# Optimization experiments

Hardware: AMD Instinct MI355X
Metric: run time of the kernel (lower is better)

Reference implementation:

```python
import jax, jax.numpy as jnp
import numpy as np

B, T, E, H, NT, NC = 256, 512, 200, 100, 100000, 5


def setup_inputs() -> dict:
    key = jax.random.key(0)
    ks = jax.random.split(key, 16)
    w = lambda i, shape: jax.random.normal(ks[i], shape, dtype=jnp.float32) * 0.05
    return {
        "txt": jax.random.randint(ks[0], (B, T), 0, NT),
        "lens": jax.random.randint(ks[1], (B,), 1, T + 1),
        "emb": w(2, (NT, E)),
        "W_ih": w(3, (3 * H, E)), "W_hh": w(4, (3 * H, H)),
        "b_ih": w(5, (3 * H,)), "b_hh": w(6, (3 * H,)),
        "W_lgr": w(7, (1, 2 * H)), "b_lgr": w(8, (1,)),
        "W_ts": w(9, (H, H)), "b_ts": w(10, (H,)),
        "W_ti": w(11, (H, H)), "b_ti": w(12, (H,)),
        "W_out": w(13, (NC, H)), "b_out": w(14, (NC,)),
    }


def reference(txt, lens, emb, W_ih, W_hh, b_ih, b_hh, W_lgr, b_lgr,
              W_ts, b_ts, W_ti, b_ti, W_out, b_out):
    bsz = txt.shape[0]
    # Embedding lookup with max_norm=1 renorm (torch nn.Embedding max_norm semantics)
    rows = emb[txt]  # (B,T,E)
    n = jnp.linalg.norm(rows, axis=-1, keepdims=True)
    emb_w = rows * jnp.where(n > 1.0, 1.0 / (n + 1e-7), 1.0)
    # eval mode: dropout is identity

    # ---- single-layer GRU (batch_first), gates in torch order r,z,n ----
    xp = emb_w @ W_ih.T + b_ih  # (B,T,3H), input projections precomputed

    def gru_step(h, x):
        hp = h @ W_hh.T + b_hh
        xr, xz, xn = jnp.split(x, 3, axis=-1)
        hr, hz, hn = jnp.split(hp, 3, axis=-1)
        r = jax.nn.sigmoid(xr + hr)
        z = jax.nn.sigmoid(xz + hz)
        ng = jnp.tanh(xn + r * hn)
        h = (1.0 - z) * ng + z * h
        return h, h

    h0 = jnp.zeros((bsz, H), jnp.float32)
    _, hs = jax.lax.scan(gru_step, h0, jnp.swapaxes(xp, 0, 1))
    rnn_out = jnp.swapaxes(hs, 0, 1)  # (B,T,H)

    # ---- cosine attention against an all-ones query ----
    inn = rnn_out / jnp.maximum(jnp.linalg.norm(rnn_out, axis=-1, keepdims=True), 1e-12)
    q = jnp.ones((bsz, H), jnp.float32)
    qn = q / jnp.maximum(jnp.linalg.norm(q, axis=-1, keepdims=True), 1e-12)
    att = jnp.einsum('bth,bh->bt', inn, qn) / H
    mask = (jnp.arange(T)[None, :] < lens[:, None]).astype(att.dtype)
    a_w = att * mask  # (B,T)

    # ---- gated-state recurrence ----
    z_all = jax.nn.relu(a_w)[..., None]          # (B,T,1)
    ti = rnn_out @ W_ti.T + b_ti                  # (B,T,H) trans_inp precomputed
    lgr_in = rnn_out @ W_lgr[:, :H].T             # (B,T,1) input half of lgr
    Wls = W_lgr[:, H:]                            # state half of lgr

    def rec_step(state, xs):
        ti_t, li_t, z_t = xs
        gate = jax.nn.sigmoid(li_t + state @ Wls.T + b_lgr)
        ns = jnp.tanh(ti_t + (gate * state) @ W_ts.T + b_ts)
        state = (1.0 - z_t) * state + z_t * ns
        return state, None

    xs = (jnp.swapaxes(ti, 0, 1), jnp.swapaxes(lgr_in, 0, 1), jnp.swapaxes(z_all, 0, 1))
    state, _ = jax.lax.scan(rec_step, jnp.zeros((bsz, H), jnp.float32), xs)
    return state @ W_out.T + b_out  # (B,NC)
```

## Files before the change

### kernel.cpp

```cpp
#include <hip/hip_runtime.h>

#define B_   256
#define T_   512
#define E_   200
#define H_   100
#define H3_  300
#define NC_  5

#define WSTRIDE 304

__device__ __forceinline__ void fma4(float4& acc, float a, const float4& w) {
    acc.x = fmaf(a, w.x, acc.x);
    acc.y = fmaf(a, w.y, acc.y);
    acc.z = fmaf(a, w.z, acc.z);
    acc.w = fmaf(a, w.w, acc.w);
}

#define KEEP4(v) asm volatile("" : "+v"((v).x), "+v"((v).y), "+v"((v).z), "+v"((v).w))

__device__ __forceinline__ void ldsbar() {
    asm volatile("s_waitcnt lgkmcnt(0)" ::: "memory");
    __builtin_amdgcn_s_barrier();
    __builtin_amdgcn_sched_barrier(0);
}

__global__ void k_pack(const float* __restrict__ W_ih, const float* __restrict__ W_ti,
                       const float* __restrict__ W_lgr,
                       float* __restrict__ wT, float* __restrict__ wcat) {
    int idx = blockIdx.x * 256 + threadIdx.x;
    if (idx < E_ * H3_) {
        int k = idx / H3_, j = idx - k * H3_;
        wT[idx] = W_ih[j * E_ + k];
    }
    int i2 = idx - E_ * H3_;
    if (i2 >= 0 && i2 < H_ * 104) {
        int k = i2 / 104, j = i2 - k * 104;
        float v = 0.0f;
        if (j < H_) v = W_ti[j * H_ + k];
        else if (j == H_) v = W_lgr[k];
        wcat[i2] = v;
    }
}

__global__ __launch_bounds__(320) void k_embgemm(
        const int* __restrict__ txt, const float* __restrict__ emb,
        const float* __restrict__ wT, const float* __restrict__ b_ih,
        float* __restrict__ xp) {
    __shared__ __align__(16) float A_lds[E_ * 36];
    __shared__ __align__(16) float W_lds[2][16 * WSTRIDE];
    __shared__ float pp_lds[10][32];
    __shared__ float scale_lds[32];

    int tid = threadIdx.x;
    int base = blockIdx.x * 32;

#pragma unroll
    for (int L = 0; L < 5; ++L) {
        int q = tid + 320 * L;
        int r = q / 50, k4 = q % 50;
        int row = txt[base + r];
        float4 v = ((const float4*)(emb + (size_t)row * E_))[k4];
        int k = k4 * 4;
        A_lds[(k + 0) * 36 + r] = v.x;
        A_lds[(k + 1) * 36 + r] = v.y;
        A_lds[(k + 2) * 36 + r] = v.z;
        A_lds[(k + 3) * 36 + r] = v.w;
    }
#pragma unroll
    for (int L = 0; L < 4; ++L) {
        int f = tid + 320 * L;
        if (f < 16 * 75) {
            int kl = f / 75, j4 = f % 75;
            float4 v = ((const float4*)wT)[kl * 75 + j4];
            *(float4*)&W_lds[0][kl * WSTRIDE + j4 * 4] = v;
        }
    }
    __syncthreads();

    {
        int r = tid % 32, s = tid / 32;
        float ss = 0.f;
        for (int k = s * 20; k < s * 20 + 20; ++k) {
            float v = A_lds[k * 36 + r];
            ss = fmaf(v, v, ss);
        }
        pp_lds[s][r] = ss;
    }
    __syncthreads();
    if (tid < 32) {
        float ss = 0.f;
#pragma unroll
        for (int s = 0; s < 10; ++s) ss += pp_lds[s][tid];
        float n = sqrtf(ss);
        scale_lds[tid] = (n > 1.0f) ? (1.0f / (n + 1e-7f)) : 1.0f;
    }

    int c = tid % 80, g = tid / 80;
    float4 acc[8];
#pragma unroll
    for (int i = 0; i < 8; ++i) acc[i] = make_float4(0.f, 0.f, 0.f, 0.f);

    const int NT = 13;
    for (int ic = 0; ic < NT; ++ic) {
        int KC = (ic == 12) ? 8 : 16;
        int cur = ic & 1;

        float4 pf0, pf1, pf2, pf3;
        int nKC = 0;
        if (ic + 1 < NT) {
            nKC = (ic + 1 == 12) ? 8 : 16;
            const float4* src = ((const float4*)wT) + (ic + 1) * 16 * 75;
            int f0 = tid;
            if (f0 < nKC * 75) pf0 = src[f0];
            int f1 = tid + 320;
            if (f1 < nKC * 75) pf1 = src[f1];
            int f2 = tid + 640;
            if (f2 < nKC * 75) pf2 = src[f2];
            int f3 = tid + 960;
            if (f3 < nKC * 75) pf3 = src[f3];
        }

        if (c < 75) {
            for (int kk = 0; kk < KC; ++kk) {
                int k = ic * 16 + kk;
                float4 wv = *(const float4*)&W_lds[cur][kk * WSTRIDE + c * 4];
                float4 a0 = *(const float4*)&A_lds[k * 36 + g * 8];
                float4 a1 = *(const float4*)&A_lds[k * 36 + g * 8 + 4];
                fma4(acc[0], a0.x, wv); fma4(acc[1], a0.y, wv);
                fma4(acc[2], a0.z, wv); fma4(acc[3], a0.w, wv);
                fma4(acc[4], a1.x, wv); fma4(acc[5], a1.y, wv);
                fma4(acc[6], a1.z, wv); fma4(acc[7], a1.w, wv);
            }
        }

        if (ic + 1 < NT) {
            int f0 = tid;
            if (f0 < nKC * 75) *(float4*)&W_lds[cur ^ 1][(f0 / 75) * WSTRIDE + (f0 % 75) * 4] = pf0;
            int f1 = tid + 320;
            if (f1 < nKC * 75) *(float4*)&W_lds[cur ^ 1][(f1 / 75) * WSTRIDE + (f1 % 75) * 4] = pf1;
            int f2 = tid + 640;
            if (f2 < nKC * 75) *(float4*)&W_lds[cur ^ 1][(f2 / 75) * WSTRIDE + (f2 % 75) * 4] = pf2;
            int f3 = tid + 960;
            if (f3 < nKC * 75) *(float4*)&W_lds[cur ^ 1][(f3 / 75) * WSTRIDE + (f3 % 75) * 4] = pf3;
        }
        ldsbar();
    }

    if (c < 75) {
        float4 bv = *(const float4*)&b_ih[c * 4];
#pragma unroll
        for (int rr = 0; rr < 8; ++rr) {
            int r = g * 8 + rr;
            float s = scale_lds[r];
            float4 res;
            res.x = fmaf(acc[rr].x, s, bv.x);
            res.y = fmaf(acc[rr].y, s, bv.y);
            res.z = fmaf(acc[rr].z, s, bv.z);
            res.w = fmaf(acc[rr].w, s, bv.w);
            *(float4*)&xp[(size_t)(base + r) * H3_ + c * 4] = res;
        }
    }
}

__global__ __launch_bounds__(640, 3)
void k_gru(
        const float* __restrict__ xp, const float* __restrict__ W_hh,
        const float* __restrict__ b_hh, float* __restrict__ rnn) {
    __shared__ __align__(16) float h_lds[104];
    __shared__ float p_lds[640];

    int tid = threadIdx.x;
    int half = (tid >= 320) ? 1 : 0;
    int j = tid - half * 320;
    int kb = half ? 48 : 0;
    int b = blockIdx.x;

    float4 w[13];
    if (j < H3_) {
        const float4* wr = (const float4*)(W_hh + (size_t)j * H_ + kb);
#pragma unroll
        for (int i = 0; i < 13; ++i) w[i] = wr[i];
        if (half) w[0] = make_float4(0.f, 0.f, 0.f, 0.f);
#pragma unroll
        for (int i = 0; i < 13; ++i) KEEP4(w[i]);
    } else {
#pragma unroll
        for (int i = 0; i < 13; ++i) w[i] = make_float4(0.f, 0.f, 0.f, 0.f);
    }

    float bhr = 0.f, bhz = 0.f, bhn = 0.f;
    if (tid < H_) { bhr = b_hh[tid]; bhz = b_hh[H_ + tid]; bhn = b_hh[2 * H_ + tid]; }

    if (tid < 104) h_lds[tid] = 0.0f;
    float hown = 0.0f;

    const float* xpb = xp + (size_t)b * T_ * H3_;
    float* rnnb = rnn + (size_t)b * T_ * H_;
    float xr = 0.f, xz = 0.f, xn = 0.f;
    if (tid < H_) { xr = xpb[tid]; xz = xpb[H_ + tid]; xn = xpb[2 * H_ + tid]; }
    __syncthreads();

    for (int t = 0; t < T_; ++t) {
        float a0 = 0.f, a1 = 0.f, a2 = 0.f, a3 = 0.f;
#pragma unroll
        for (int i = 0; i < 13; ++i) {
            float4 hv = *(const float4*)&h_lds[kb + i * 4];
            a0 = fmaf(w[i].x, hv.x, a0);
            a1 = fmaf(w[i].y, hv.y, a1);
            a2 = fmaf(w[i].z, hv.z, a2);
            a3 = fmaf(w[i].w, hv.w, a3);
        }
        float ownp = (a0 + a1) + (a2 + a3);
        if (j < H3_) p_lds[tid] = ownp;
        float nxr = 0.f, nxz = 0.f, nxn = 0.f;
        if (tid < H_ && t + 1 < T_) {
            const float* xq = xpb + (size_t)(t + 1) * H3_;
            nxr = xq[tid]; nxz = xq[H_ + tid]; nxn = xq[2 * H_ + tid];
        }
        ldsbar();
        if (tid < H_) {
            float hr = ownp             + p_lds[320 + tid] + bhr;
            float hz = p_lds[100 + tid] + p_lds[420 + tid] + bhz;
            float hn = p_lds[200 + tid] + p_lds[520 + tid] + bhn;
            float r = 1.0f / (1.0f + expf(-(xr + hr)));
            float z = 1.0f / (1.0f + expf(-(xz + hz)));
            float ng = tanhf(xn + r * hn);
            float hnew = (1.0f - z) * ng + z * hown;
            hown = hnew;
            h_lds[tid] = hnew;
            rnnb[(size_t)t * H_ + tid] = hnew;
            xr = nxr; xz = nxz; xn = nxn;
        }
        ldsbar();
    }
}

__global__ __launch_bounds__(256) void k_post(
        const float* __restrict__ rnn, const float* __restrict__ wcat,
        const float* __restrict__ b_ti, const int* __restrict__ lens,
        float* __restrict__ ti, float* __restrict__ lgr, float* __restrict__ zr) {
    __shared__ __align__(16) float A_lds[H_ * 72];
    __shared__ __align__(16) float W_lds[H_ * 112];

    int tid = threadIdx.x;
    int base = blockIdx.x * 64;

    for (int idx = tid; idx < 64 * H_; idx += 256) {
        int r = idx / H_, k = idx - r * H_;
        A_lds[k * 72 + r] = rnn[(size_t)(base + r) * H_ + k];
    }
    for (int idx = tid; idx < H_ * 104; idx += 256) {
        int k = idx / 104, jj = idx - k * 104;
        W_lds[k * 112 + jj] = wcat[idx];
    }
    __syncthreads();

    if (tid < 64) {
        float ss = 0.f, sm = 0.f;
        for (int k = 0; k < H_; ++k) {
            float v = A_lds[k * 72 + tid];
            ss = fmaf(v, v, ss); sm += v;
        }
        int row = base + tid;
        int bb = row >> 9, tt = row & 511;
        float att = sm / (fmaxf(sqrtf(ss), 1e-12f) * 1000.0f);
        zr[row] = (tt < lens[bb]) ? fmaxf(att, 0.0f) : 0.0f;
    }

    int c = tid % 32, g = tid / 32;
    float4 acc[8];
#pragma unroll
    for (int i = 0; i < 8; ++i) acc[i] = make_float4(0.f, 0.f, 0.f, 0.f);

    if (c < 26) {
        for (int k = 0; k < H_; ++k) {
            float4 wv = *(const float4*)&W_lds[k * 112 + c * 4];
            float4 a0 = *(const float4*)&A_lds[k * 72 + g * 8];
            float4 a1 = *(const float4*)&A_lds[k * 72 + g * 8 + 4];
            fma4(acc[0], a0.x, wv); fma4(acc[1], a0.y, wv);
            fma4(acc[2], a0.z, wv); fma4(acc[3], a0.w, wv);
            fma4(acc[4], a1.x, wv); fma4(acc[5], a1.y, wv);
            fma4(acc[6], a1.z, wv); fma4(acc[7], a1.w, wv);
        }
    }

    if (c < 25) {
        float4 bv = *(const float4*)&b_ti[c * 4];
#pragma unroll
        for (int rr = 0; rr < 8; ++rr) {
            int row = base + g * 8 + rr;
            float4 res;
            res.x = acc[rr].x + bv.x; res.y = acc[rr].y + bv.y;
            res.z = acc[rr].z + bv.z; res.w = acc[rr].w + bv.w;
            *(float4*)&ti[(size_t)row * H_ + c * 4] = res;
        }
    } else if (c == 25) {
#pragma unroll
        for (int rr = 0; rr < 8; ++rr) {
            int row = base + g * 8 + rr;
            lgr[row] = acc[rr].x;
        }
    }
}

__global__ __launch_bounds__(256, 1)
void k_rec(
        const float* __restrict__ ti, const float* __restrict__ lgr,
        const float* __restrict__ zr,
        const float* __restrict__ W_ts, const float* __restrict__ b_ts,
        const float* __restrict__ W_lgr, const float* __restrict__ b_lgr,
        const float* __restrict__ W_out, const float* __restrict__ b_out,
        float* __restrict__ out) {
    __shared__ __align__(16) float sA[104];
    __shared__ __align__(16) float sB[104];
    __shared__ float p_lds[256];
    __shared__ float red[2][2];

    int tid = threadIdx.x;
    int half = (tid >= 128) ? 1 : 0;
    int j = tid - half * 128;
    int kb = half ? 48 : 0;
    int b = blockIdx.x;

    float4 w[13];
    if (j < H_) {
        const float4* wr = (const float4*)(W_ts + (size_t)j * H_ + kb);
#pragma unroll
        for (int i = 0; i < 13; ++i) w[i] = wr[i];
        if (half) w[0] = make_float4(0.f, 0.f, 0.f, 0.f);
#pragma unroll
        for (int i = 0; i < 13; ++i) KEEP4(w[i]);
    } else {
#pragma unroll
        for (int i = 0; i < 13; ++i) w[i] = make_float4(0.f, 0.f, 0.f, 0.f);
    }

    float bts = 0.f, wlj = 0.f;
    if (tid < H_) { bts = b_ts[tid]; wlj = W_lgr[H_ + tid]; }
    float blg = b_lgr[0];
    if (tid < 104) sA[tid] = 0.0f;
    if (tid < 4) ((float*)red)[tid] = 0.0f;
    float sown = 0.0f;

    size_t rb = (size_t)b * T_;
    float tiv = 0.f, zt = 0.f, lt = 0.f;
    if (tid < H_) tiv = ti[rb * H_ + tid];
    zt = zr[rb]; lt = lgr[rb];
    __syncthreads();

    float* rd = sA;
    float* wrb = sB;
    for (int t = 0; t < T_; ++t) {
        float a0 = 0.f, a1 = 0.f, a2 = 0.f, a3 = 0.f;
#pragma unroll
        for (int i = 0; i < 13; ++i) {
            float4 s4 = *(const float4*)&rd[kb + i * 4];
            a0 = fmaf(w[i].x, s4.x, a0); a1 = fmaf(w[i].y, s4.y, a1);
            a2 = fmaf(w[i].z, s4.z, a2); a3 = fmaf(w[i].w, s4.w, a3);
        }
        float ownp = (a0 + a1) + (a2 + a3);
        if (half && j < H_) p_lds[tid] = ownp;
        float ntiv = 0.f, nzt = 0.f, nlt = 0.f;
        if (t + 1 < T_) {
            if (tid < H_) ntiv = ti[(rb + t + 1) * H_ + tid];
            nzt = zr[rb + t + 1]; nlt = lgr[rb + t + 1];
        }
        ldsbar();
        float dot = red[t & 1][0] + red[t & 1][1];
        float part = 0.0f;
        if (tid < H_) {
            float sv = ownp + p_lds[128 + tid];
            float gate = 1.0f / (1.0f + expf(-(lt + dot + blg)));
            float ns = tanhf(tiv + gate * sv + bts);
            float snew = (1.0f - zt) * sown + zt * ns;
            sown = snew;
            wrb[tid] = snew;
            part = wlj * snew;
        }
        tiv = ntiv; zt = nzt; lt = nlt;
#pragma unroll
        for (int off = 1; off < 64; off <<= 1) part += __shfl_xor(part, off, 64);
        if ((tid & 63) == 0 && tid < 128) red[(t + 1) & 1][tid >> 6] = part;
        ldsbar();
        float* tmp = rd; rd = wrb; wrb = tmp;
    }

    if (tid < NC_) {
        float o = b_out[tid];
        for (int k = 0; k < H_; ++k) o = fmaf(rd[k], W_out[tid * H_ + k], o);
        out[b * NC_ + tid] = o;
    }
}

extern "C" void kernel_launch(void* const* d_in, const int* in_sizes, int n_in,
                              void* d_out, int out_size, void* d_ws, size_t ws_size,
                              hipStream_t stream) {
    const int*   txt   = (const int*)d_in[0];
    const int*   lens  = (const int*)d_in[1];
    const float* emb   = (const float*)d_in[2];
    const float* W_ih  = (const float*)d_in[3];
    const float* W_hh  = (const float*)d_in[4];
    const float* b_ih  = (const float*)d_in[5];
    const float* b_hh  = (const float*)d_in[6];
    const float* W_lgr = (const float*)d_in[7];
    const float* b_lgr = (const float*)d_in[8];
    const float* W_ts  = (const float*)d_in[9];
    const float* b_ts  = (const float*)d_in[10];
    const float* W_ti  = (const float*)d_in[11];
    const float* b_ti  = (const float*)d_in[12];
    const float* W_out = (const float*)d_in[13];
    const float* b_out = (const float*)d_in[14];

    float* ws   = (float*)d_ws;
    float* xp   = ws;
    float* rnn  = xp + 39321600;
    float* lgrv = rnn + 13107200;
    float* zrv  = lgrv + 131072;
    float* wT   = zrv + 131072;
    float* wcat = wT + 60000;
    float* ti   = xp;

    float* out = (float*)d_out;

    k_pack<<<276, 256, 0, stream>>>(W_ih, W_ti, W_lgr, wT, wcat);
    k_embgemm<<<4096, 320, 0, stream>>>(txt, emb, wT, b_ih, xp);
    k_gru<<<256, 640, 0, stream>>>(xp, W_hh, b_hh, rnn);
    k_post<<<2048, 256, 0, stream>>>(rnn, wcat, b_ti, lens, ti, lgrv, zrv);
    k_rec<<<256, 256, 0, stream>>>(ti, lgrv, zrv, W_ts, b_ts, W_lgr, b_lgr,
                                   W_out, b_out, out);
}
```

Measured before the change: 1.528 ms.

## Split GRU and recurrence dot products three ways and broadcast state via readlane

Both sequential recurrences now split the hidden-size reduction across three thread groups of 36/32/32 elements instead of two halves of roughly 52, using 960 and 384 threads per block. Each lane loads a single element of the state from LDS once per step, and the dot product pulls each operand with v_readlane as a scalar instead of doing repeated float4 LDS reads. The aim is a shorter per-step critical path in these latency-bound scans. In exchange there are more waves per barrier, a third partial sum to combine, and possible readlane hazard stalls. The k_rec state double buffer is replaced by a single LDS buffer.

```diff
diff --git a/kernel.cpp b/kernel.cpp
--- a/kernel.cpp
+++ b/kernel.cpp
@@ -22,6 +22,23 @@
     asm volatile("s_waitcnt lgkmcnt(0)" ::: "memory");
     __builtin_amdgcn_s_barrier();
     __builtin_amdgcn_sched_barrier(0);
+}
+
+__device__ __forceinline__ float rlane(float v, int l) {
+    return __uint_as_float(__builtin_amdgcn_readlane(__float_as_uint(v), (unsigned)l));
+}
+
+template<int N4>
+__device__ __forceinline__ float dotseg(const float4 (&w)[9], float hreg) {
+    float a0 = 0.f, a1 = 0.f, a2 = 0.f, a3 = 0.f;
+#pragma unroll
+    for (int q = 0; q < N4; ++q) {
+        a0 = fmaf(w[q].x, rlane(hreg, 4 * q + 0), a0);
+        a1 = fmaf(w[q].y, rlane(hreg, 4 * q + 1), a1);
+        a2 = fmaf(w[q].z, rlane(hreg, 4 * q + 2), a2);
+        a3 = fmaf(w[q].w, rlane(hreg, 4 * q + 3), a3);
+    }
+    return (a0 + a1) + (a2 + a3);
 }
 
 __global__ void k_pack(const float* __restrict__ W_ih, const float* __restrict__ W_ti,
@@ -162,56 +179,48 @@
     }
 }
 
-__global__ __launch_bounds__(640, 3)
+__global__ __launch_bounds__(960)
+__attribute__((amdgpu_waves_per_eu(1, 4)))
 void k_gru(
         const float* __restrict__ xp, const float* __restrict__ W_hh,
         const float* __restrict__ b_hh, float* __restrict__ rnn) {
-    __shared__ __align__(16) float h_lds[104];
-    __shared__ float p_lds[640];
+    __shared__ float h_lds[104];
+    __shared__ float p_lds[960];
 
     int tid = threadIdx.x;
-    int half = (tid >= 320) ? 1 : 0;
-    int j = tid - half * 320;
-    int kb = half ? 48 : 0;
+    int lane = tid & 63;
+    int third = tid / 320;
+    int j = tid - third * 320;
+    int kb = (third == 0) ? 0 : (third == 1 ? 36 : 68);
+    int seg = (third == 0) ? 36 : 32;
+    int seg4 = (third == 0) ? 9 : 8;
     int b = blockIdx.x;
 
-    float4 w[13];
+    float4 w4[9];
+#pragma unroll
+    for (int q = 0; q < 9; ++q) w4[q] = make_float4(0.f, 0.f, 0.f, 0.f);
     if (j < H3_) {
         const float4* wr = (const float4*)(W_hh + (size_t)j * H_ + kb);
 #pragma unroll
-        for (int i = 0; i < 13; ++i) w[i] = wr[i];
-        if (half) w[0] = make_float4(0.f, 0.f, 0.f, 0.f);
-#pragma unroll
-        for (int i = 0; i < 13; ++i) KEEP4(w[i]);
-    } else {
-#pragma unroll
-        for (int i = 0; i < 13; ++i) w[i] = make_float4(0.f, 0.f, 0.f, 0.f);
-    }
+        for (int q = 0; q < 9; ++q) if (q < seg4) w4[q] = wr[q];
+    }
+#pragma unroll
+    for (int q = 0; q < 9; ++q) KEEP4(w4[q]);
 
     float bhr = 0.f, bhz = 0.f, bhn = 0.f;
     if (tid < H_) { bhr = b_hh[tid]; bhz = b_hh[H_ + tid]; bhn = b_hh[2 * H_ + tid]; }
-
-    if (tid < 104) h_lds[tid] = 0.0f;
-    float hown = 0.0f;
 
     const float* xpb = xp + (size_t)b * T_ * H3_;
     float* rnnb = rnn + (size_t)b * T_ * H_;
     float xr = 0.f, xz = 0.f, xn = 0.f;
     if (tid < H_) { xr = xpb[tid]; xz = xpb[H_ + tid]; xn = xpb[2 * H_ + tid]; }
-    __syncthreads();
+
+    float hreg = 0.f;
+    float hown = 0.f;
 
     for (int t = 0; t < T_; ++t) {
-        float a0 = 0.f, a1 = 0.f, a2 = 0.f, a3 = 0.f;
-#pragma unroll
-        for (int i = 0; i < 13; ++i) {
-            float4 hv = *(const float4*)&h_lds[kb + i * 4];
-            a0 = fmaf(w[i].x, hv.x, a0);
-            a1 = fmaf(w[i].y, hv.y, a1);
-            a2 = fmaf(w[i].z, hv.z, a2);
-            a3 = fmaf(w[i].w, hv.w, a3);
-        }
-        float ownp = (a0 + a1) + (a2 + a3);
-        if (j < H3_) p_lds[tid] = ownp;
+        float p = (third == 0) ? dotseg<9>(w4, hreg) : dotseg<8>(w4, hreg);
+        if (j < H3_) p_lds[tid] = p;
         float nxr = 0.f, nxz = 0.f, nxn = 0.f;
         if (tid < H_ && t + 1 < T_) {
             const float* xq = xpb + (size_t)(t + 1) * H3_;
@@ -219,9 +228,9 @@
         }
         ldsbar();
         if (tid < H_) {
-            float hr = ownp             + p_lds[320 + tid] + bhr;
-            float hz = p_lds[100 + tid] + p_lds[420 + tid] + bhz;
-            float hn = p_lds[200 + tid] + p_lds[520 + tid] + bhn;
+            float hr = p + p_lds[320 + tid] + p_lds[640 + tid] + bhr;
+            float hz = p_lds[100 + tid] + p_lds[420 + tid] + p_lds[740 + tid] + bhz;
+            float hn = p_lds[200 + tid] + p_lds[520 + tid] + p_lds[840 + tid] + bhn;
             float r = 1.0f / (1.0f + expf(-(xr + hr)));
             float z = 1.0f / (1.0f + expf(-(xz + hz)));
             float ng = tanhf(xn + r * hn);
@@ -232,6 +241,7 @@
             xr = nxr; xz = nxz; xn = nxn;
         }
         ldsbar();
+        hreg = (lane < seg) ? h_lds[kb + lane] : 0.f;
     }
 }
 
@@ -303,7 +313,8 @@
     }
 }
 
-__global__ __launch_bounds__(256, 1)
+__global__ __launch_bounds__(384)
+__attribute__((amdgpu_waves_per_eu(1, 4)))
 void k_rec(
         const float* __restrict__ ti, const float* __restrict__ lgr,
         const float* __restrict__ zr,
@@ -311,55 +322,45 @@
         const float* __restrict__ W_lgr, const float* __restrict__ b_lgr,
         const float* __restrict__ W_out, const float* __restrict__ b_out,
         float* __restrict__ out) {
-    __shared__ __align__(16) float sA[104];
-    __shared__ __align__(16) float sB[104];
-    __shared__ float p_lds[256];
+    __shared__ float st_lds[104];
+    __shared__ float p_lds[384];
     __shared__ float red[2][2];
 
     int tid = threadIdx.x;
-    int half = (tid >= 128) ? 1 : 0;
-    int j = tid - half * 128;
-    int kb = half ? 48 : 0;
+    int lane = tid & 63;
+    int third = tid / 128;
+    int j = tid - third * 128;
+    int kb = (third == 0) ? 0 : (third == 1 ? 36 : 68);
+    int seg = (third == 0) ? 36 : 32;
+    int seg4 = (third == 0) ? 9 : 8;
     int b = blockIdx.x;
 
-    float4 w[13];
+    float4 w4[9];
+#pragma unroll
+    for (int q = 0; q < 9; ++q) w4[q] = make_float4(0.f, 0.f, 0.f, 0.f);
     if (j < H_) {
         const float4* wr = (const float4*)(W_ts + (size_t)j * H_ + kb);
 #pragma unroll
-        for (int i = 0; i < 13; ++i) w[i] = wr[i];
-        if (half) w[0] = make_float4(0.f, 0.f, 0.f, 0.f);
-#pragma unroll
-        for (int i = 0; i < 13; ++i) KEEP4(w[i]);
-    } else {
-#pragma unroll
-        for (int i = 0; i < 13; ++i) w[i] = make_float4(0.f, 0.f, 0.f, 0.f);
-    }
+        for (int q = 0; q < 9; ++q) if (q < seg4) w4[q] = wr[q];
+    }
+#pragma unroll
+    for (int q = 0; q < 9; ++q) KEEP4(w4[q]);
 
     float bts = 0.f, wlj = 0.f;
     if (tid < H_) { bts = b_ts[tid]; wlj = W_lgr[H_ + tid]; }
     float blg = b_lgr[0];
-    if (tid < 104) sA[tid] = 0.0f;
     if (tid < 4) ((float*)red)[tid] = 0.0f;
     float sown = 0.0f;
+    float sreg = 0.0f;
 
     size_t rb = (size_t)b * T_;
     float tiv = 0.f, zt = 0.f, lt = 0.f;
     if (tid < H_) tiv = ti[rb * H_ + tid];
     zt = zr[rb]; lt = lgr[rb];
-    __syncthreads();
-
-    float* rd = sA;
-    float* wrb = sB;
+
     for (int t = 0; t < T_; ++t) {
-        float a0 = 0.f, a1 = 0.f, a2 = 0.f, a3 = 0.f;
-#pragma unroll
-        for (int i = 0; i < 13; ++i) {
-            float4 s4 = *(const float4*)&rd[kb + i * 4];
-            a0 = fmaf(w[i].x, s4.x, a0); a1 = fmaf(w[i].y, s4.y, a1);
-            a2 = fmaf(w[i].z, s4.z, a2); a3 = fmaf(w[i].w, s4.w, a3);
-        }
-        float ownp = (a0 + a1) + (a2 + a3);
-        if (half && j < H_) p_lds[tid] = ownp;
+        float p = (third == 0) ? dotseg<9>(w4, sreg) : dotseg<8>(w4, sreg);
+        if (j < H_) p_lds[tid] = p;
         float ntiv = 0.f, nzt = 0.f, nlt = 0.f;
         if (t + 1 < T_) {
             if (tid < H_) ntiv = ti[(rb + t + 1) * H_ + tid];
@@ -369,25 +370,27 @@
         float dot = red[t & 1][0] + red[t & 1][1];
         float part = 0.0f;
         if (tid < H_) {
-            float sv = ownp + p_lds[128 + tid];
+            float sv = p + p_lds[128 + tid] + p_lds[256 + tid];
             float gate = 1.0f / (1.0f + expf(-(lt + dot + blg)));
             float ns = tanhf(tiv + gate * sv + bts);
             float snew = (1.0f - zt) * sown + zt * ns;
             sown = snew;
-            wrb[tid] = snew;
+            st_lds[tid] = snew;
             part = wlj * snew;
         }
         tiv = ntiv; zt = nzt; lt = nlt;
-#pragma unroll
-        for (int off = 1; off < 64; off <<= 1) part += __shfl_xor(part, off, 64);
-        if ((tid & 63) == 0 && tid < 128) red[(t + 1) & 1][tid >> 6] = part;
+        if (tid < 128) {
+#pragma unroll
+            for (int off = 1; off < 64; off <<= 1) part += __shfl_xor(part, off, 64);
+            if ((tid & 63) == 0) red[(t + 1) & 1][tid >> 6] = part;
+        }
         ldsbar();
-        float* tmp = rd; rd = wrb; wrb = tmp;
+        sreg = (lane < seg) ? st_lds[kb + lane] : 0.f;
     }
 
     if (tid < NC_) {
         float o = b_out[tid];
-        for (int k = 0; k < H_; ++k) o = fmaf(rd[k], W_out[tid * H_ + k], o);
+        for (int k = 0; k < H_; ++k) o = fmaf(st_lds[k], W_out[tid * H_ + k], o);
         out[b * NC_ + tid] = o;
     }
 }
@@ -424,8 +427,8 @@
 
     k_pack<<<276, 256, 0, stream>>>(W_ih, W_ti, W_lgr, wT, wcat);
     k_embgemm<<<4096, 320, 0, stream>>>(txt, emb, wT, b_ih, xp);
-    k_gru<<<256, 640, 0, stream>>>(xp, W_hh, b_hh, rnn);
+    k_gru<<<256, 960, 0, stream>>>(xp, W_hh, b_hh, rnn);
     k_post<<<2048, 256, 0, stream>>>(rnn, wcat, b_ti, lens, ti, lgrv, zrv);
-    k_rec<<<256, 256, 0, stream>>>(ti, lgrv, zrv, W_ts, b_ts, W_lgr, b_lgr,
+    k_rec<<<256, 384, 0, stream>>>(ti, lgrv, zrv, W_ts, b_ts, W_lgr, b_lgr,
                                    W_out, b_out, out);
 }
```

After: 1.441 ms. 5.7% less time.

## Move recurrent weights to LDS and drop split-K partial-sum barrier in GRU and rec

Applied to the files above, without the earlier changes.

Both recurrent kernels stop holding weight rows in registers split across two half-blocks. Each thread now reads its full weight row from a padded shared-memory copy. This halves the thread count per block and, in k_rec, removes one barrier per timestep because no cross-half partial-sum exchange is needed. The trade is many more LDS reads per step (weights plus state) and longer per-thread dot products on the serial critical path.

```diff
diff --git a/kernel.cpp b/kernel.cpp
--- a/kernel.cpp
+++ b/kernel.cpp
@@ -8,6 +8,7 @@
 #define NC_  5
 
 #define WSTRIDE 304
+#define RSTR   108
 
 __device__ __forceinline__ void fma4(float4& acc, float a, const float4& w) {
     acc.x = fmaf(a, w.x, acc.x);
@@ -15,8 +16,6 @@
     acc.z = fmaf(a, w.z, acc.z);
     acc.w = fmaf(a, w.w, acc.w);
 }
-
-#define KEEP4(v) asm volatile("" : "+v"((v).x), "+v"((v).y), "+v"((v).z), "+v"((v).w))
 
 __device__ __forceinline__ void ldsbar() {
     asm volatile("s_waitcnt lgkmcnt(0)" ::: "memory");
@@ -162,35 +161,25 @@
     }
 }
 
-__global__ __launch_bounds__(640, 3)
+__global__ __launch_bounds__(320, 1)
 void k_gru(
         const float* __restrict__ xp, const float* __restrict__ W_hh,
         const float* __restrict__ b_hh, float* __restrict__ rnn) {
+    __shared__ __align__(16) float Wl[H3_ * RSTR];
     __shared__ __align__(16) float h_lds[104];
-    __shared__ float p_lds[640];
+    __shared__ float hp_lds[H3_];
 
     int tid = threadIdx.x;
-    int half = (tid >= 320) ? 1 : 0;
-    int j = tid - half * 320;
-    int kb = half ? 48 : 0;
     int b = blockIdx.x;
 
-    float4 w[13];
-    if (j < H3_) {
-        const float4* wr = (const float4*)(W_hh + (size_t)j * H_ + kb);
-#pragma unroll
-        for (int i = 0; i < 13; ++i) w[i] = wr[i];
-        if (half) w[0] = make_float4(0.f, 0.f, 0.f, 0.f);
-#pragma unroll
-        for (int i = 0; i < 13; ++i) KEEP4(w[i]);
-    } else {
-#pragma unroll
-        for (int i = 0; i < 13; ++i) w[i] = make_float4(0.f, 0.f, 0.f, 0.f);
+    for (int idx = tid; idx < 7500; idx += 320) {
+        int j = idx / 25, q = idx - j * 25;
+        float4 v = ((const float4*)(W_hh + (size_t)j * H_))[q];
+        *(float4*)&Wl[j * RSTR + q * 4] = v;
     }
 
     float bhr = 0.f, bhz = 0.f, bhn = 0.f;
     if (tid < H_) { bhr = b_hh[tid]; bhz = b_hh[H_ + tid]; bhn = b_hh[2 * H_ + tid]; }
-
     if (tid < 104) h_lds[tid] = 0.0f;
     float hown = 0.0f;
 
@@ -200,18 +189,21 @@
     if (tid < H_) { xr = xpb[tid]; xz = xpb[H_ + tid]; xn = xpb[2 * H_ + tid]; }
     __syncthreads();
 
+    const float* wr = &Wl[tid * RSTR];
     for (int t = 0; t < T_; ++t) {
-        float a0 = 0.f, a1 = 0.f, a2 = 0.f, a3 = 0.f;
-#pragma unroll
-        for (int i = 0; i < 13; ++i) {
-            float4 hv = *(const float4*)&h_lds[kb + i * 4];
-            a0 = fmaf(w[i].x, hv.x, a0);
-            a1 = fmaf(w[i].y, hv.y, a1);
-            a2 = fmaf(w[i].z, hv.z, a2);
-            a3 = fmaf(w[i].w, hv.w, a3);
-        }
-        float ownp = (a0 + a1) + (a2 + a3);
-        if (j < H3_) p_lds[tid] = ownp;
+        if (tid < H3_) {
+            float a0 = 0.f, a1 = 0.f, a2 = 0.f, a3 = 0.f;
+#pragma unroll
+            for (int q = 0; q < 25; ++q) {
+                float4 wv = *(const float4*)&wr[q * 4];
+                float4 hv = *(const float4*)&h_lds[q * 4];
+                a0 = fmaf(wv.x, hv.x, a0);
+                a1 = fmaf(wv.y, hv.y, a1);
+                a2 = fmaf(wv.z, hv.z, a2);
+                a3 = fmaf(wv.w, hv.w, a3);
+            }
+            hp_lds[tid] = (a0 + a1) + (a2 + a3);
+        }
         float nxr = 0.f, nxz = 0.f, nxn = 0.f;
         if (tid < H_ && t + 1 < T_) {
             const float* xq = xpb + (size_t)(t + 1) * H3_;
@@ -219,9 +211,9 @@
         }
         ldsbar();
         if (tid < H_) {
-            float hr = ownp             + p_lds[320 + tid] + bhr;
-            float hz = p_lds[100 + tid] + p_lds[420 + tid] + bhz;
-            float hn = p_lds[200 + tid] + p_lds[520 + tid] + bhn;
+            float hr = hp_lds[tid] + bhr;
+            float hz = hp_lds[H_ + tid] + bhz;
+            float hn = hp_lds[2 * H_ + tid] + bhn;
             float r = 1.0f / (1.0f + expf(-(xr + hr)));
             float z = 1.0f / (1.0f + expf(-(xz + hz)));
             float ng = tanhf(xn + r * hn);
@@ -303,7 +295,7 @@
     }
 }
 
-__global__ __launch_bounds__(256, 1)
+__global__ __launch_bounds__(128, 1)
 void k_rec(
         const float* __restrict__ ti, const float* __restrict__ lgr,
         const float* __restrict__ zr,
@@ -311,28 +303,19 @@
         const float* __restrict__ W_lgr, const float* __restrict__ b_lgr,
         const float* __restrict__ W_out, const float* __restrict__ b_out,
         float* __restrict__ out) {
+    __shared__ __align__(16) float Wl[H_ * RSTR];
     __shared__ __align__(16) float sA[104];
     __shared__ __align__(16) float sB[104];
-    __shared__ float p_lds[256];
     __shared__ float red[2][2];
 
     int tid = threadIdx.x;
-    int half = (tid >= 128) ? 1 : 0;
-    int j = tid - half * 128;
-    int kb = half ? 48 : 0;
     int b = blockIdx.x;
-
-    float4 w[13];
-    if (j < H_) {
-        const float4* wr = (const float4*)(W_ts + (size_t)j * H_ + kb);
-#pragma unroll
-        for (int i = 0; i < 13; ++i) w[i] = wr[i];
-        if (half) w[0] = make_float4(0.f, 0.f, 0.f, 0.f);
-#pragma unroll
-        for (int i = 0; i < 13; ++i) KEEP4(w[i]);
-    } else {
-#pragma unroll
-        for (int i = 0; i < 13; ++i) w[i] = make_float4(0.f, 0.f, 0.f, 0.f);
+    int wave = tid >> 6;
+
+    for (int idx = tid; idx < 2500; idx += 128) {
+        int j = idx / 25, q = idx - j * 25;
+        float4 v = ((const float4*)(W_ts + (size_t)j * H_))[q];
+        *(float4*)&Wl[j * RSTR + q * 4] = v;
     }
 
     float bts = 0.f, wlj = 0.f;
@@ -348,28 +331,30 @@
     zt = zr[rb]; lt = lgr[rb];
     __syncthreads();
 
+    const float* wr = &Wl[tid * RSTR];
     float* rd = sA;
     float* wrb = sB;
     for (int t = 0; t < T_; ++t) {
-        float a0 = 0.f, a1 = 0.f, a2 = 0.f, a3 = 0.f;
-#pragma unroll
-        for (int i = 0; i < 13; ++i) {
-            float4 s4 = *(const float4*)&rd[kb + i * 4];
-            a0 = fmaf(w[i].x, s4.x, a0); a1 = fmaf(w[i].y, s4.y, a1);
-            a2 = fmaf(w[i].z, s4.z, a2); a3 = fmaf(w[i].w, s4.w, a3);
-        }
-        float ownp = (a0 + a1) + (a2 + a3);
-        if (half && j < H_) p_lds[tid] = ownp;
+        float sv = 0.f;
+        if (tid < H_) {
+            float a0 = 0.f, a1 = 0.f, a2 = 0.f, a3 = 0.f;
+#pragma unroll
+            for (int q = 0; q < 25; ++q) {
+                float4 wv = *(const float4*)&wr[q * 4];
+                float4 s4 = *(const float4*)&rd[q * 4];
+                a0 = fmaf(wv.x, s4.x, a0); a1 = fmaf(wv.y, s4.y, a1);
+                a2 = fmaf(wv.z, s4.z, a2); a3 = fmaf(wv.w, s4.w, a3);
+            }
+            sv = (a0 + a1) + (a2 + a3);
+        }
         float ntiv = 0.f, nzt = 0.f, nlt = 0.f;
         if (t + 1 < T_) {
             if (tid < H_) ntiv = ti[(rb + t + 1) * H_ + tid];
             nzt = zr[rb + t + 1]; nlt = lgr[rb + t + 1];
         }
-        ldsbar();
         float dot = red[t & 1][0] + red[t & 1][1];
         float part = 0.0f;
         if (tid < H_) {
-            float sv = ownp + p_lds[128 + tid];
             float gate = 1.0f / (1.0f + expf(-(lt + dot + blg)));
             float ns = tanhf(tiv + gate * sv + bts);
             float snew = (1.0f - zt) * sown + zt * ns;
@@ -380,7 +365,7 @@
         tiv = ntiv; zt = nzt; lt = nlt;
 #pragma unroll
         for (int off = 1; off < 64; off <<= 1) part += __shfl_xor(part, off, 64);
-        if ((tid & 63) == 0 && tid < 128) red[(t + 1) & 1][tid >> 6] = part;
+        if ((tid & 63) == 0) red[(t + 1) & 1][wave] = part;
         ldsbar();
         float* tmp = rd; rd = wrb; wrb = tmp;
     }
@@ -424,8 +409,8 @@
 
     k_pack<<<276, 256, 0, stream>>>(W_ih, W_ti, W_lgr, wT, wcat);
     k_embgemm<<<4096, 320, 0, stream>>>(txt, emb, wT, b_ih, xp);
-    k_gru<<<256, 640, 0, stream>>>(xp, W_hh, b_hh, rnn);
+    k_gru<<<256, 320, 0, stream>>>(xp, W_hh, b_hh, rnn);
     k_post<<<2048, 256, 0, stream>>>(rnn, wcat, b_ti, lens, ti, lgrv, zrv);
-    k_rec<<<256, 256, 0, stream>>>(ti, lgrv, zrv, W_ts, b_ts, W_lgr, b_lgr,
+    k_rec<<<256, 128, 0, stream>>>(ti, lgrv, zrv, W_ts, b_ts, W_lgr, b_lgr,
                                    W_out, b_out, out);
 }
```

Result: slower. 2.119 ms (+38.7%).
